# Kernel optimization log

Hardware: AMD Instinct MI355X
Metric: run time of the kernel (lower is better)

The kernel has to match this reference:

```python
import jax, jax.numpy as jnp
import numpy as np

SEQ = 2048
D_MODEL = 2048
N_HEAD = 16
D_QK = 128
D_V = 128
THETA = 10000.0


def setup_inputs() -> dict:
    key = jax.random.key(0)
    kx, kq, kk, kv, ko = jax.random.split(key, 5)
    x = jax.random.normal(kx, (SEQ, D_MODEL), dtype=jnp.float32)
    q = jax.random.normal(kq, (N_HEAD, D_MODEL, D_QK), dtype=jnp.float32)
    k = jax.random.normal(kk, (N_HEAD, D_MODEL, D_QK), dtype=jnp.float32)
    v = jax.random.normal(kv, (N_HEAD, D_MODEL, D_V), dtype=jnp.float32)
    o = jax.random.normal(ko, (N_HEAD, D_V, D_MODEL), dtype=jnp.float32)
    theta_factor = jnp.asarray(THETA, dtype=jnp.float32)
    return {"x": x, "q": q, "k": k, "v": v, "o": o, "theta_factor": theta_factor}


def _rope_embed(x, d_qk, theta_factor):
    # x: [..., S, d]. Rotate-half RoPE with frequencies theta^(-i/d_rope),
    # then scale by d_qk^(-1/4) so q.k gets the usual 1/sqrt(d_qk).
    S, d = x.shape[-2], x.shape[-1]
    d_rope = d // 2
    rates = theta_factor ** (-jnp.arange(d_rope, dtype=x.dtype) / d_rope)  # [d_rope]
    ang = jnp.arange(S, dtype=x.dtype)[:, None] * rates[None, :]           # [S, d_rope]
    sin, cos = jnp.sin(ang), jnp.cos(ang)
    x1, x2 = x[..., :d_rope], x[..., d_rope:]
    y = jnp.concatenate([cos * x1 - sin * x2, sin * x1 + cos * x2], axis=-1)
    return y * (d_qk ** -0.25)


def reference(x, q, k, v, o, theta_factor):
    # x: [S, D]; q,k: [H, D, d_qk]; v: [H, D, d_v]; o: [H, d_v, D]
    S = x.shape[0]
    d_qk = q.shape[2]
    qs = jnp.einsum('sd,hde->hse', x, q)   # [H, S, d_qk]
    ks = jnp.einsum('sd,hde->hse', x, k)   # [H, S, d_qk]
    vs = jnp.einsum('sd,hde->hse', x, v)   # [H, S, d_v]
    rq = _rope_embed(qs, d_qk, theta_factor)
    rk = _rope_embed(ks, d_qk, theta_factor)
    scores = jnp.einsum('hse,hte->hst', rq, rk)  # [H, S, S]
    causal = jnp.tril(jnp.ones((S, S), dtype=bool))
    scores = jnp.where(causal[None], scores, -jnp.inf)
    w = jax.nn.softmax(scores, axis=-1)
    y = jnp.einsum('hst,hte->hse', w, vs)        # [H, S, d_v]
    z = jnp.einsum('hse,hed->sd', y, o)          # [S, D] (sum over heads)
    return z
```

## Files before the change

kernel.cpp:

```cpp
#include <hip/hip_runtime.h>
#include <hip/hip_bf16.h>

#define SEQ 2048
#define DM  2048
#define NH  16
#define DE  128
#define DR  64
#define LDT 72
#define LDK 136

typedef __attribute__((ext_vector_type(8))) short bf16x8;
typedef __attribute__((ext_vector_type(4))) float f32x4;

#define VMCNT_WAIT(n) asm volatile("s_waitcnt vmcnt(" #n ")" ::: "memory")
#define CFENCE() asm volatile("" ::: "memory")

__device__ __forceinline__ unsigned short f2bf(float f) {
  unsigned u = __float_as_uint(f);
  u += 0x7fff + ((u >> 16) & 1);
  return (unsigned short)(u >> 16);
}
__device__ __forceinline__ float bf2f(unsigned short h) {
  return __uint_as_float((unsigned)h << 16);
}

__device__ __forceinline__ void gld16(const unsigned short* g, unsigned short* l) {
  __builtin_amdgcn_global_load_lds(
      (const __attribute__((address_space(1))) unsigned int*)g,
      (__attribute__((address_space(3))) unsigned int*)l, 16, 0, 0);
}

__global__ void k_split(const float* __restrict__ in, unsigned short* __restrict__ hi,
                        unsigned short* __restrict__ lo, int n4) {
  int i = blockIdx.x * blockDim.x + threadIdx.x;
  int stride = gridDim.x * blockDim.x;
  for (int idx = i; idx < n4; idx += stride) {
    float4 v = ((const float4*)in)[idx];
    ushort4 h, l;
    h.x = f2bf(v.x); l.x = f2bf(v.x - bf2f(h.x));
    h.y = f2bf(v.y); l.y = f2bf(v.y - bf2f(h.y));
    h.z = f2bf(v.z); l.z = f2bf(v.z - bf2f(h.z));
    h.w = f2bf(v.w); l.w = f2bf(v.w - bf2f(h.w));
    ((ushort4*)hi)[idx] = h;
    ((ushort4*)lo)[idx] = l;
  }
}

__global__ void k_transpose_split(const float* __restrict__ in, unsigned short* __restrict__ hi,
                                  unsigned short* __restrict__ lo, int rows, int cols) {
  __shared__ float tile[32][33];
  size_t bo = (size_t)blockIdx.z * rows * cols;
  int r0 = blockIdx.y * 32, c0 = blockIdx.x * 32;
  int tx = threadIdx.x, ty = threadIdx.y;
  #pragma unroll
  for (int i = 0; i < 32; i += 8)
    tile[ty + i][tx] = in[bo + (size_t)(r0 + ty + i) * cols + (c0 + tx)];
  __syncthreads();
  #pragma unroll
  for (int i = 0; i < 32; i += 8) {
    float v = tile[tx][ty + i];
    unsigned short h = f2bf(v);
    size_t oidx = bo + (size_t)(c0 + ty + i) * rows + (r0 + tx);
    hi[oidx] = h;
    lo[oidx] = f2bf(v - bf2f(h));
  }
}

__global__ void k_transpose_one(const float* __restrict__ in, unsigned short* __restrict__ out,
                                int rows, int cols) {
  __shared__ float tile[32][33];
  size_t bo = (size_t)blockIdx.z * rows * cols;
  int r0 = blockIdx.y * 32, c0 = blockIdx.x * 32;
  int tx = threadIdx.x, ty = threadIdx.y;
  #pragma unroll
  for (int i = 0; i < 32; i += 8)
    tile[ty + i][tx] = in[bo + (size_t)(r0 + ty + i) * cols + (c0 + tx)];
  __syncthreads();
  #pragma unroll
  for (int i = 0; i < 32; i += 8)
    out[bo + (size_t)(c0 + ty + i) * rows + (r0 + tx)] = f2bf(tile[tx][ty + i]);
}

__global__ void k_rope_tables(const float* __restrict__ theta_p,
                              float* __restrict__ cost, float* __restrict__ sint) {
  int s = blockIdx.x, j = threadIdx.x;
  float theta = theta_p[0];
  float rate = powf(theta, -(float)j * (1.0f / (float)DR));
  float ang = (float)s * rate;
  cost[s * DR + j] = cosf(ang);
  sint[s * DR + j] = sinf(ang);
}

__launch_bounds__(256)
__global__ void k_projall(const unsigned short* __restrict__ xh, const unsigned short* __restrict__ xl,
                          const unsigned short* __restrict__ wqh, const unsigned short* __restrict__ wql,
                          const unsigned short* __restrict__ wkh, const unsigned short* __restrict__ wkl,
                          const unsigned short* __restrict__ wvh,
                          unsigned short* __restrict__ rqh, unsigned short* __restrict__ rql,
                          unsigned short* __restrict__ rkh, unsigned short* __restrict__ rkl,
                          unsigned short* __restrict__ vstt,
                          const float* __restrict__ cost, const float* __restrict__ sint) {
  __shared__ unsigned short Ahs[2][128 * 32];
  __shared__ unsigned short Als[2][128 * 32];
  __shared__ unsigned short Bhs[2][128 * 32];
  __shared__ unsigned short Bls[2][128 * 32];
  int mt = blockIdx.x;
  int mat = blockIdx.y >> 4, h = blockIdx.y & 15;
  bool split = (mat < 2);
  const unsigned short* wph = (mat == 0 ? wqh : (mat == 1 ? wkh : wvh)) + (size_t)h * DE * DM;
  const unsigned short* wpl = (mat == 0 ? wql : wkl) + (size_t)h * DE * DM;
  int m0 = mt * 128;
  int tid = threadIdx.x, lane = tid & 63, wid = tid >> 6;
  int wr = wid >> 1, wc = wid & 1;

  f32x4 zero = {0.f, 0.f, 0.f, 0.f};
  f32x4 acc[4][4];
  #pragma unroll
  for (int i = 0; i < 4; ++i)
    #pragma unroll
    for (int j = 0; j < 4; ++j) acc[i][j] = zero;

  auto STAGE = [&](int buf, int k0) {
    #pragma unroll
    for (int p = 0; p < 2; ++p) {
      int r = p * 64 + wid * 16 + (lane >> 2);
      int c = ((lane & 3) ^ ((r >> 1) & 3)) * 8;
      int ld = r * 32 + (lane & 3) * 8;
      gld16(&xh[(size_t)(m0 + r) * DM + k0 + c], &Ahs[buf][ld]);
      gld16(&wph[(size_t)r * DM + k0 + c], &Bhs[buf][ld]);
      if (split) {
        gld16(&xl[(size_t)(m0 + r) * DM + k0 + c], &Als[buf][ld]);
        gld16(&wpl[(size_t)r * DM + k0 + c], &Bls[buf][ld]);
      }
    }
  };

  const int NT = DM / 32;
  STAGE(0, 0);
  STAGE(1, 32);
  int cl_ = lane & 15;
  int chunk = lane >> 4;
  #pragma unroll 2
  for (int t = 0; t < NT; ++t) {
    int buf = t & 1;
    if (split) { VMCNT_WAIT(8); } else { VMCNT_WAIT(4); }
    __builtin_amdgcn_s_barrier();
    CFENCE();
    bf16x8 ah[4], al[4], bh[4], bl[4];
    #pragma unroll
    for (int mf = 0; mf < 4; ++mf) {
      int row = wr * 64 + mf * 16 + cl_;
      int off = row * 32 + ((chunk ^ ((row >> 1) & 3)) * 8);
      ah[mf] = *(const bf16x8*)&Ahs[buf][off];
      if (split) al[mf] = *(const bf16x8*)&Als[buf][off];
    }
    #pragma unroll
    for (int nf = 0; nf < 4; ++nf) {
      int nfi = wc * 2 + (nf & 1) + (nf >> 1) * 4;
      int row = nfi * 16 + cl_;
      int off = row * 32 + ((chunk ^ ((row >> 1) & 3)) * 8);
      bh[nf] = *(const bf16x8*)&Bhs[buf][off];
      if (split) bl[nf] = *(const bf16x8*)&Bls[buf][off];
    }
    if (split) {
      #pragma unroll
      for (int mf = 0; mf < 4; ++mf)
        #pragma unroll
        for (int nf = 0; nf < 4; ++nf) {
          acc[mf][nf] = __builtin_amdgcn_mfma_f32_16x16x32_bf16(ah[mf], bh[nf], acc[mf][nf], 0, 0, 0);
          acc[mf][nf] = __builtin_amdgcn_mfma_f32_16x16x32_bf16(al[mf], bh[nf], acc[mf][nf], 0, 0, 0);
          acc[mf][nf] = __builtin_amdgcn_mfma_f32_16x16x32_bf16(ah[mf], bl[nf], acc[mf][nf], 0, 0, 0);
        }
    } else {
      #pragma unroll
      for (int mf = 0; mf < 4; ++mf)
        #pragma unroll
        for (int nf = 0; nf < 4; ++nf)
          acc[mf][nf] = __builtin_amdgcn_mfma_f32_16x16x32_bf16(ah[mf], bh[nf], acc[mf][nf], 0, 0, 0);
    }
    CFENCE();
    __builtin_amdgcn_s_barrier();
    int kn = (t + 2 < NT) ? (t + 2) * 32 : (NT - 1) * 32;
    STAGE(buf, kn);
  }
  VMCNT_WAIT(0);

  int cl = lane & 15, rl = (lane >> 4) * 4;
  if (mat == 2) {
    #pragma unroll
    for (int mf = 0; mf < 4; ++mf)
      #pragma unroll
      for (int nf = 0; nf < 4; ++nf) {
        int nfi = wc * 2 + (nf & 1) + (nf >> 1) * 4;
        #pragma unroll
        for (int j = 0; j < 4; ++j) {
          int s = m0 + wr * 64 + mf * 16 + rl + j;
          int e = nfi * 16 + cl;
          vstt[((size_t)h * DE + e) * SEQ + s] = f2bf(acc[mf][nf][j]);
        }
      }
  } else {
    unsigned short* oh = (mat == 0) ? rqh : rkh;
    unsigned short* ol = (mat == 0) ? rql : rkl;
    const float qsc = 0.2973017787506803f;
    #pragma unroll
    for (int mf = 0; mf < 4; ++mf)
      #pragma unroll
      for (int nf = 0; nf < 2; ++nf)
        #pragma unroll
        for (int j = 0; j < 4; ++j) {
          int s = m0 + wr * 64 + mf * 16 + rl + j;
          int e = wc * 32 + (nf & 1) * 16 + cl;
          float x1 = acc[mf][nf][j];
          float x2 = acc[mf][nf + 2][j];
          float c  = cost[s * DR + e];
          float sn = sint[s * DR + e];
          float v1 = (c * x1 - sn * x2) * qsc;
          float v2 = (sn * x1 + c * x2) * qsc;
          size_t i1 = ((size_t)h * SEQ + s) * DE + e;
          size_t i2 = i1 + DR;
          unsigned short h1 = f2bf(v1), h2 = f2bf(v2);
          oh[i1] = h1; ol[i1] = f2bf(v1 - bf2f(h1));
          oh[i2] = h2; ol[i2] = f2bf(v2 - bf2f(h2));
        }
  }
}

#define LOADKV(t0)                                                        \
  pkh0 = *(const int4*)&Kh[(size_t)((t0) + sk_r     ) * DE + sk_c];       \
  pkh1 = *(const int4*)&Kh[(size_t)((t0) + sk_r + 16) * DE + sk_c];       \
  pkh2 = *(const int4*)&Kh[(size_t)((t0) + sk_r + 32) * DE + sk_c];       \
  pkh3 = *(const int4*)&Kh[(size_t)((t0) + sk_r + 48) * DE + sk_c];       \
  pkl0 = *(const int4*)&Kl[(size_t)((t0) + sk_r     ) * DE + sk_c];       \
  pkl1 = *(const int4*)&Kl[(size_t)((t0) + sk_r + 16) * DE + sk_c];       \
  pkl2 = *(const int4*)&Kl[(size_t)((t0) + sk_r + 32) * DE + sk_c];       \
  pkl3 = *(const int4*)&Kl[(size_t)((t0) + sk_r + 48) * DE + sk_c];       \
  pvv0 = *(const int4*)&Vt[(size_t)(sv_r     ) * SEQ + (t0) + sv_c];      \
  pvv1 = *(const int4*)&Vt[(size_t)(sv_r + 32) * SEQ + (t0) + sv_c];      \
  pvv2 = *(const int4*)&Vt[(size_t)(sv_r + 64) * SEQ + (t0) + sv_c];      \
  pvv3 = *(const int4*)&Vt[(size_t)(sv_r + 96) * SEQ + (t0) + sv_c];

#define STOREKV()                                                         \
  *(int4*)&Khi[(sk_r     ) * LDK + sk_c] = pkh0;                          \
  *(int4*)&Khi[(sk_r + 16) * LDK + sk_c] = pkh1;                          \
  *(int4*)&Khi[(sk_r + 32) * LDK + sk_c] = pkh2;                          \
  *(int4*)&Khi[(sk_r + 48) * LDK + sk_c] = pkh3;                          \
  *(int4*)&Klo[(sk_r     ) * LDK + sk_c] = pkl0;                          \
  *(int4*)&Klo[(sk_r + 16) * LDK + sk_c] = pkl1;                          \
  *(int4*)&Klo[(sk_r + 32) * LDK + sk_c] = pkl2;                          \
  *(int4*)&Klo[(sk_r + 48) * LDK + sk_c] = pkl3;                          \
  *(int4*)&Vtl[(sv_r     ) * LDT + sv_c] = pvv0;                          \
  *(int4*)&Vtl[(sv_r + 32) * LDT + sv_c] = pvv1;                          \
  *(int4*)&Vtl[(sv_r + 64) * LDT + sv_c] = pvv2;                          \
  *(int4*)&Vtl[(sv_r + 96) * LDT + sv_c] = pvv3;

__launch_bounds__(256, 2)
__global__ void k_attn(const unsigned short* __restrict__ rqh, const unsigned short* __restrict__ rql,
                       const unsigned short* __restrict__ rkh, const unsigned short* __restrict__ rkl,
                       const unsigned short* __restrict__ vstt,
                       unsigned short* __restrict__ yb) {
  __shared__ unsigned short Khi[64 * LDK];
  __shared__ unsigned short Klo[64 * LDK];
  __shared__ unsigned short Vtl[128 * LDT];
  __shared__ unsigned short Pl[64 * LDT];
  int bid = blockIdx.x;
  int g = bid >> 4;
  int qt = (g < 16) ? (31 - g) : (g - 16);
  int h  = bid & 15;
  int m0 = qt * 64;
  int tid = threadIdx.x, lane = tid & 63, wid = tid >> 6;
  const unsigned short* Qh = rqh + (size_t)h * SEQ * DE;
  const unsigned short* Ql = rql + (size_t)h * SEQ * DE;
  const unsigned short* Kh = rkh + (size_t)h * SEQ * DE;
  const unsigned short* Kl = rkl + (size_t)h * SEQ * DE;
  const unsigned short* Vt = vstt + (size_t)h * DE * SEQ;
  int cl = lane & 15, hi = lane >> 4;

  bf16x8 qfh[4], qfl[4];
  {
    int qrow = m0 + wid * 16 + cl;
    #pragma unroll
    for (int ks = 0; ks < 4; ++ks) {
      qfh[ks] = *(const bf16x8*)&Qh[(size_t)qrow * DE + ks * 32 + hi * 8];
      qfl[ks] = *(const bf16x8*)&Ql[(size_t)qrow * DE + ks * 32 + hi * 8];
    }
  }

  f32x4 zero = {0.f, 0.f, 0.f, 0.f};
  f32x4 acc[8];
  #pragma unroll
  for (int nf = 0; nf < 8; ++nf) acc[nf] = zero;
  float mrow[4], lrow[4];
  #pragma unroll
  for (int j = 0; j < 4; ++j) { mrow[j] = -3e38f; lrow[j] = 0.f; }

  int sk_r = tid >> 4, sk_c = (tid & 15) * 8;
  int sv_r = tid >> 3, sv_c = (tid & 7) * 8;

  int4 pkh0, pkh1, pkh2, pkh3, pkl0, pkl1, pkl2, pkl3, pvv0, pvv1, pvv2, pvv3;

  int ntiles = qt + 1;
  LOADKV(0)
  for (int t = 0; t < ntiles; ++t) {
    int t0 = t * 64;
    STOREKV()
    __syncthreads();
    if (t + 1 < ntiles) { LOADKV(t0 + 64) }

    f32x4 sacc[4];
    #pragma unroll
    for (int tf = 0; tf < 4; ++tf) sacc[tf] = zero;
    __builtin_amdgcn_s_setprio(1);
    #pragma unroll
    for (int ks = 0; ks < 4; ++ks) {
      int kk = ks * 32 + hi * 8;
      #pragma unroll
      for (int tf = 0; tf < 4; ++tf) {
        int r = (tf * 16 + cl) * LDK + kk;
        bf16x8 bh = *(const bf16x8*)&Khi[r];
        bf16x8 bl = *(const bf16x8*)&Klo[r];
        sacc[tf] = __builtin_amdgcn_mfma_f32_16x16x32_bf16(qfh[ks], bh, sacc[tf], 0, 0, 0);
        sacc[tf] = __builtin_amdgcn_mfma_f32_16x16x32_bf16(qfl[ks], bh, sacc[tf], 0, 0, 0);
        sacc[tf] = __builtin_amdgcn_mfma_f32_16x16x32_bf16(qfh[ks], bl, sacc[tf], 0, 0, 0);
      }
    }
    __builtin_amdgcn_s_setprio(0);
    if (t == ntiles - 1) {
      int sb = m0 + wid * 16 + hi * 4;
      #pragma unroll
      for (int tf = 0; tf < 4; ++tf) {
        int tc = t0 + tf * 16 + cl;
        #pragma unroll
        for (int j = 0; j < 4; ++j)
          if (tc > sb + j) sacc[tf][j] = -3e38f;
      }
    }
    #pragma unroll
    for (int j = 0; j < 4; ++j) {
      float mx = fmaxf(fmaxf(sacc[0][j], sacc[1][j]), fmaxf(sacc[2][j], sacc[3][j]));
      mx = fmaxf(mx, __shfl_xor(mx, 1));
      mx = fmaxf(mx, __shfl_xor(mx, 2));
      mx = fmaxf(mx, __shfl_xor(mx, 4));
      mx = fmaxf(mx, __shfl_xor(mx, 8));
      float mnew = fmaxf(mrow[j], mx);
      float sc = __expf(mrow[j] - mnew);
      float sum = 0.f;
      #pragma unroll
      for (int tf = 0; tf < 4; ++tf) {
        float p = __expf(sacc[tf][j] - mnew);
        sacc[tf][j] = p;
        sum += p;
      }
      sum += __shfl_xor(sum, 1);
      sum += __shfl_xor(sum, 2);
      sum += __shfl_xor(sum, 4);
      sum += __shfl_xor(sum, 8);
      lrow[j] = lrow[j] * sc + sum;
      mrow[j] = mnew;
      #pragma unroll
      for (int nf = 0; nf < 8; ++nf) acc[nf][j] *= sc;
    }
    #pragma unroll
    for (int tf = 0; tf < 4; ++tf)
      #pragma unroll
      for (int j = 0; j < 4; ++j)
        Pl[(wid * 16 + hi * 4 + j) * LDT + tf * 16 + cl] = f2bf(sacc[tf][j]);
    __builtin_amdgcn_s_setprio(1);
    #pragma unroll
    for (int ks = 0; ks < 2; ++ks) {
      int kk = ks * 32 + hi * 8;
      bf16x8 a = *(const bf16x8*)&Pl[(wid * 16 + cl) * LDT + kk];
      #pragma unroll
      for (int nf = 0; nf < 8; ++nf) {
        bf16x8 b = *(const bf16x8*)&Vtl[(nf * 16 + cl) * LDT + kk];
        acc[nf] = __builtin_amdgcn_mfma_f32_16x16x32_bf16(a, b, acc[nf], 0, 0, 0);
      }
    }
    __builtin_amdgcn_s_setprio(0);
    __syncthreads();
  }

  #pragma unroll
  for (int j = 0; j < 4; ++j) {
    float inv = 1.0f / lrow[j];
    #pragma unroll
    for (int nf = 0; nf < 8; ++nf) acc[nf][j] *= inv;
  }
  #pragma unroll
  for (int nf = 0; nf < 8; ++nf)
    #pragma unroll
    for (int j = 0; j < 4; ++j) {
      int s = m0 + wid * 16 + hi * 4 + j;
      int e = nf * 16 + cl;
      yb[(size_t)s * DM + h * DE + e] = f2bf(acc[nf][j]);
    }
}

__launch_bounds__(256)
__global__ void k_out(const unsigned short* __restrict__ yb,
                      const unsigned short* __restrict__ otb,
                      float* __restrict__ z) {
  __shared__ unsigned short Ahs[2][128 * 32];
  __shared__ unsigned short Bhs[2][128 * 32];
  int m0 = blockIdx.x * 128, n0 = blockIdx.y * 128;
  int tid = threadIdx.x, lane = tid & 63, wid = tid >> 6;
  int wr = wid >> 1, wc = wid & 1;
  f32x4 zero = {0.f, 0.f, 0.f, 0.f};
  f32x4 acc[4][4];
  #pragma unroll
  for (int i = 0; i < 4; ++i)
    #pragma unroll
    for (int j = 0; j < 4; ++j) acc[i][j] = zero;

  auto STAGE = [&](int buf, int k0) {
    #pragma unroll
    for (int p = 0; p < 2; ++p) {
      int r = p * 64 + wid * 16 + (lane >> 2);
      int c = ((lane & 3) ^ ((r >> 1) & 3)) * 8;
      int ld = r * 32 + (lane & 3) * 8;
      gld16(&yb[(size_t)(m0 + r) * DM + k0 + c], &Ahs[buf][ld]);
      gld16(&otb[(size_t)(n0 + r) * DM + k0 + c], &Bhs[buf][ld]);
    }
  };

  const int NT = DM / 32;
  STAGE(0, 0);
  STAGE(1, 32);
  int cl_ = lane & 15;
  int chunk = lane >> 4;
  #pragma unroll 2
  for (int t = 0; t < NT; ++t) {
    int buf = t & 1;
    VMCNT_WAIT(4);
    __builtin_amdgcn_s_barrier();
    CFENCE();
    bf16x8 a[4], b[4];
    #pragma unroll
    for (int mf = 0; mf < 4; ++mf) {
      int row = wr * 64 + mf * 16 + cl_;
      a[mf] = *(const bf16x8*)&Ahs[buf][row * 32 + ((chunk ^ ((row >> 1) & 3)) * 8)];
    }
    #pragma unroll
    for (int nf = 0; nf < 4; ++nf) {
      int nfi = wc * 2 + (nf & 1) + (nf >> 1) * 4;
      int row = nfi * 16 + cl_;
      b[nf] = *(const bf16x8*)&Bhs[buf][row * 32 + ((chunk ^ ((row >> 1) & 3)) * 8)];
    }
    #pragma unroll
    for (int mf = 0; mf < 4; ++mf)
      #pragma unroll
      for (int nf = 0; nf < 4; ++nf)
        acc[mf][nf] = __builtin_amdgcn_mfma_f32_16x16x32_bf16(a[mf], b[nf], acc[mf][nf], 0, 0, 0);
    CFENCE();
    __builtin_amdgcn_s_barrier();
    int kn = (t + 2 < NT) ? (t + 2) * 32 : (NT - 1) * 32;
    STAGE(buf, kn);
  }
  VMCNT_WAIT(0);

  int cl = lane & 15, rl = (lane >> 4) * 4;
  #pragma unroll
  for (int mf = 0; mf < 4; ++mf)
    #pragma unroll
    for (int nf = 0; nf < 4; ++nf) {
      int nfi = wc * 2 + (nf & 1) + (nf >> 1) * 4;
      #pragma unroll
      for (int j = 0; j < 4; ++j) {
        int s = m0 + wr * 64 + mf * 16 + rl + j;
        int d = n0 + nfi * 16 + cl;
        z[(size_t)s * DM + d] = acc[mf][nf][j];
      }
    }
}

extern "C" void kernel_launch(void* const* d_in, const int* in_sizes, int n_in,
                              void* d_out, int out_size, void* d_ws, size_t ws_size,
                              hipStream_t stream) {
  const float* x  = (const float*)d_in[0];
  const float* q  = (const float*)d_in[1];
  const float* k  = (const float*)d_in[2];
  const float* v  = (const float*)d_in[3];
  const float* o  = (const float*)d_in[4];
  const float* th = (const float*)d_in[5];
  float* z = (float*)d_out;
  char* ws = (char*)d_ws;
  const size_t MB = 1024 * 1024;
  unsigned short* xh  = (unsigned short*)(ws);
  unsigned short* xl  = (unsigned short*)(ws + 8 * MB);
  unsigned short* wqh = (unsigned short*)(ws + 16 * MB);
  unsigned short* wql = (unsigned short*)(ws + 24 * MB);
  unsigned short* wkh = (unsigned short*)(ws + 32 * MB);
  unsigned short* wkl = (unsigned short*)(ws + 40 * MB);
  unsigned short* wvh = (unsigned short*)(ws + 48 * MB);
  unsigned short* rqh = (unsigned short*)(ws + 56 * MB);
  unsigned short* rql = (unsigned short*)(ws + 64 * MB);
  unsigned short* rkh = (unsigned short*)(ws + 72 * MB);
  unsigned short* rkl = (unsigned short*)(ws + 80 * MB);
  unsigned short* vst = (unsigned short*)(ws + 88 * MB);
  float* cost = (float*)(ws + 96 * MB);
  float* sint = (float*)(ws + 96 * MB + 512 * 1024);
  unsigned short* yb  = (unsigned short*)(ws + 16 * MB);
  unsigned short* otb = (unsigned short*)(ws + 24 * MB);

  dim3 tb(32, 8);
  k_rope_tables<<<SEQ, DR, 0, stream>>>(th, cost, sint);
  k_split<<<2048, 256, 0, stream>>>(x, xh, xl, SEQ * DM / 4);
  k_transpose_split<<<dim3(DE / 32, DM / 32, NH), tb, 0, stream>>>(q, wqh, wql, DM, DE);
  k_transpose_split<<<dim3(DE / 32, DM / 32, NH), tb, 0, stream>>>(k, wkh, wkl, DM, DE);
  k_transpose_one<<<dim3(DE / 32, DM / 32, NH), tb, 0, stream>>>(v, wvh, DM, DE);
  k_projall<<<dim3(16, 48), 256, 0, stream>>>(xh, xl, wqh, wql, wkh, wkl, wvh,
                                              rqh, rql, rkh, rkl, vst, cost, sint);
  k_transpose_one<<<dim3(DM / 32, (NH * DE) / 32, 1), tb, 0, stream>>>(o, otb, NH * DE, DM);
  k_attn<<<512, 256, 0, stream>>>(rqh, rql, rkh, rkl, vst, yb);
  k_out<<<dim3(16, 16), 256, 0, stream>>>(yb, otb, z);
}
```

Before: 318.2 us.

## Use 256x256 tiles with 8 waves and phased MFMA/LDS schedule in projection

The QKV projection GEMM moves from 128x128 tiles with 4 waves (768 blocks) to 256x256 tiles with 8 waves (192 blocks). Each wave now computes a 128x64 sub-tile in four phases that interleave LDS fragment reads, next-tile global prefetch and MFMA bursts, with barriers between phases and raised wave priority during the MFMA bursts. The larger tiles cut redundant global and LDS traffic per flop. In exchange the launch has only 192 blocks for 256 CUs, the loop waits for all outstanding loads each step and adds many barriers, and the 128 KB of LDS may not fit two blocks per CU.

```diff
diff --git a/kernel.cpp b/kernel.cpp
--- a/kernel.cpp
+++ b/kernel.cpp
@@ -91,8 +91,8 @@
   sint[s * DR + j] = sinf(ang);
 }
 
-__launch_bounds__(256)
-__global__ void k_projall(const unsigned short* __restrict__ xh, const unsigned short* __restrict__ xl,
+__launch_bounds__(512, 2)
+__global__ void k_proj256(const unsigned short* __restrict__ xh, const unsigned short* __restrict__ xl,
                           const unsigned short* __restrict__ wqh, const unsigned short* __restrict__ wql,
                           const unsigned short* __restrict__ wkh, const unsigned short* __restrict__ wkl,
                           const unsigned short* __restrict__ wvh,
@@ -100,103 +100,115 @@
                           unsigned short* __restrict__ rkh, unsigned short* __restrict__ rkl,
                           unsigned short* __restrict__ vstt,
                           const float* __restrict__ cost, const float* __restrict__ sint) {
-  __shared__ unsigned short Ahs[2][128 * 32];
-  __shared__ unsigned short Als[2][128 * 32];
-  __shared__ unsigned short Bhs[2][128 * 32];
-  __shared__ unsigned short Bls[2][128 * 32];
-  int mt = blockIdx.x;
-  int mat = blockIdx.y >> 4, h = blockIdx.y & 15;
+  __shared__ unsigned short Ahs[2][256 * 32];
+  __shared__ unsigned short Als[2][256 * 32];
+  __shared__ unsigned short Bhs[2][256 * 32];
+  __shared__ unsigned short Bls[2][256 * 32];
+  int bid = blockIdx.x;
+  int mat = bid >> 6;
+  int mt = (bid >> 3) & 7, nt = bid & 7;
   bool split = (mat < 2);
-  const unsigned short* wph = (mat == 0 ? wqh : (mat == 1 ? wkh : wvh)) + (size_t)h * DE * DM;
-  const unsigned short* wpl = (mat == 0 ? wql : wkl) + (size_t)h * DE * DM;
-  int m0 = mt * 128;
+  const unsigned short* wh = (mat == 0 ? wqh : (mat == 1 ? wkh : wvh));
+  const unsigned short* wl = (mat == 0 ? wql : wkl);
+  int m0 = mt * 256, n0 = nt * 256;
   int tid = threadIdx.x, lane = tid & 63, wid = tid >> 6;
-  int wr = wid >> 1, wc = wid & 1;
+  int wr = wid >> 2, wc = wid & 3;
+  int cl_ = lane & 15, chunk = lane >> 4;
+  int sr = tid >> 2, ss = tid & 3;
 
   f32x4 zero = {0.f, 0.f, 0.f, 0.f};
-  f32x4 acc[4][4];
-  #pragma unroll
-  for (int i = 0; i < 4; ++i)
+  f32x4 acc[8][4];
+  #pragma unroll
+  for (int i = 0; i < 8; ++i)
     #pragma unroll
     for (int j = 0; j < 4; ++j) acc[i][j] = zero;
 
-  auto STAGE = [&](int buf, int k0) {
-    #pragma unroll
-    for (int p = 0; p < 2; ++p) {
-      int r = p * 64 + wid * 16 + (lane >> 2);
-      int c = ((lane & 3) ^ ((r >> 1) & 3)) * 8;
-      int ld = r * 32 + (lane & 3) * 8;
-      gld16(&xh[(size_t)(m0 + r) * DM + k0 + c], &Ahs[buf][ld]);
-      gld16(&wph[(size_t)r * DM + k0 + c], &Bhs[buf][ld]);
-      if (split) {
-        gld16(&xl[(size_t)(m0 + r) * DM + k0 + c], &Als[buf][ld]);
-        gld16(&wpl[(size_t)r * DM + k0 + c], &Bls[buf][ld]);
-      }
-    }
-  };
-
+#define STAGEP(bufv, k0, p) {                                              \
+    int r_ = sr + (p) * 128;                                               \
+    int c_ = (ss ^ ((r_ >> 1) & 3)) * 8;                                   \
+    int ld_ = r_ * 32 + ss * 8;                                            \
+    gld16(&xh[(size_t)(m0 + r_) * DM + (k0) + c_], &Ahs[bufv][ld_]);       \
+    gld16(&wh[(size_t)(n0 + r_) * DM + (k0) + c_], &Bhs[bufv][ld_]);       \
+    if (split) {                                                           \
+      gld16(&xl[(size_t)(m0 + r_) * DM + (k0) + c_], &Als[bufv][ld_]);     \
+      gld16(&wl[(size_t)(n0 + r_) * DM + (k0) + c_], &Bls[bufv][ld_]);     \
+    }                                                                      \
+  }
+#define RA(dh, dl, mfv) {                                                  \
+    int row_ = wr * 128 + (mfv) * 16 + cl_;                                \
+    int off_ = row_ * 32 + ((chunk ^ ((row_ >> 1) & 3)) * 8);              \
+    dh = *(const bf16x8*)&Ahs[buf][off_];                                  \
+    if (split) dl = *(const bf16x8*)&Als[buf][off_];                       \
+  }
+#define RB(dh, dl, nfv) {                                                  \
+    int row_ = ((nfv) * 4 + wc) * 16 + cl_;                                \
+    int off_ = row_ * 32 + ((chunk ^ ((row_ >> 1) & 3)) * 8);              \
+    dh = *(const bf16x8*)&Bhs[buf][off_];                                  \
+    if (split) dl = *(const bf16x8*)&Bls[buf][off_];                       \
+  }
+#define MM3(a_, ahv, alv, bhv, blv)                                        \
+    a_ = __builtin_amdgcn_mfma_f32_16x16x32_bf16(ahv, bhv, a_, 0, 0, 0);   \
+    a_ = __builtin_amdgcn_mfma_f32_16x16x32_bf16(alv, bhv, a_, 0, 0, 0);   \
+    a_ = __builtin_amdgcn_mfma_f32_16x16x32_bf16(ahv, blv, a_, 0, 0, 0);
+#define MM1(a_, ahv, bhv)                                                  \
+    a_ = __builtin_amdgcn_mfma_f32_16x16x32_bf16(ahv, bhv, a_, 0, 0, 0);
+#define PH_MFMA(mA, mB, nA, nB)                                            \
+    __builtin_amdgcn_s_setprio(1);                                         \
+    if (split) {                                                           \
+      MM3(acc[mA][nA], ah0, al0, bh0, bl0) MM3(acc[mA][nB], ah0, al0, bh1, bl1) \
+      MM3(acc[mA+1][nA], ah1, al1, bh0, bl0) MM3(acc[mA+1][nB], ah1, al1, bh1, bl1) \
+      MM3(acc[mA+2][nA], ah2, al2, bh0, bl0) MM3(acc[mA+2][nB], ah2, al2, bh1, bl1) \
+      MM3(acc[mA+3][nA], ah3, al3, bh0, bl0) MM3(acc[mA+3][nB], ah3, al3, bh1, bl1) \
+    } else {                                                               \
+      MM1(acc[mA][nA], ah0, bh0) MM1(acc[mA][nB], ah0, bh1)                \
+      MM1(acc[mA+1][nA], ah1, bh0) MM1(acc[mA+1][nB], ah1, bh1)            \
+      MM1(acc[mA+2][nA], ah2, bh0) MM1(acc[mA+2][nB], ah2, bh1)            \
+      MM1(acc[mA+3][nA], ah3, bh0) MM1(acc[mA+3][nB], ah3, bh1)            \
+    }                                                                      \
+    __builtin_amdgcn_s_setprio(0);
+#define PBAR() CFENCE(); __builtin_amdgcn_s_barrier(); CFENCE();
+
+  STAGEP(0, 0, 0)
+  STAGEP(0, 0, 1)
   const int NT = DM / 32;
-  STAGE(0, 0);
-  STAGE(1, 32);
-  int cl_ = lane & 15;
-  int chunk = lane >> 4;
-  #pragma unroll 2
   for (int t = 0; t < NT; ++t) {
     int buf = t & 1;
-    if (split) { VMCNT_WAIT(8); } else { VMCNT_WAIT(4); }
-    __builtin_amdgcn_s_barrier();
-    CFENCE();
-    bf16x8 ah[4], al[4], bh[4], bl[4];
-    #pragma unroll
-    for (int mf = 0; mf < 4; ++mf) {
-      int row = wr * 64 + mf * 16 + cl_;
-      int off = row * 32 + ((chunk ^ ((row >> 1) & 3)) * 8);
-      ah[mf] = *(const bf16x8*)&Ahs[buf][off];
-      if (split) al[mf] = *(const bf16x8*)&Als[buf][off];
-    }
-    #pragma unroll
-    for (int nf = 0; nf < 4; ++nf) {
-      int nfi = wc * 2 + (nf & 1) + (nf >> 1) * 4;
-      int row = nfi * 16 + cl_;
-      int off = row * 32 + ((chunk ^ ((row >> 1) & 3)) * 8);
-      bh[nf] = *(const bf16x8*)&Bhs[buf][off];
-      if (split) bl[nf] = *(const bf16x8*)&Bls[buf][off];
-    }
-    if (split) {
-      #pragma unroll
-      for (int mf = 0; mf < 4; ++mf)
-        #pragma unroll
-        for (int nf = 0; nf < 4; ++nf) {
-          acc[mf][nf] = __builtin_amdgcn_mfma_f32_16x16x32_bf16(ah[mf], bh[nf], acc[mf][nf], 0, 0, 0);
-          acc[mf][nf] = __builtin_amdgcn_mfma_f32_16x16x32_bf16(al[mf], bh[nf], acc[mf][nf], 0, 0, 0);
-          acc[mf][nf] = __builtin_amdgcn_mfma_f32_16x16x32_bf16(ah[mf], bl[nf], acc[mf][nf], 0, 0, 0);
-        }
-    } else {
-      #pragma unroll
-      for (int mf = 0; mf < 4; ++mf)
-        #pragma unroll
-        for (int nf = 0; nf < 4; ++nf)
-          acc[mf][nf] = __builtin_amdgcn_mfma_f32_16x16x32_bf16(ah[mf], bh[nf], acc[mf][nf], 0, 0, 0);
-    }
-    CFENCE();
-    __builtin_amdgcn_s_barrier();
-    int kn = (t + 2 < NT) ? (t + 2) * 32 : (NT - 1) * 32;
-    STAGE(buf, kn);
+    VMCNT_WAIT(0);
+    PBAR();
+    bf16x8 ah0, ah1, ah2, ah3, al0, al1, al2, al3, bh0, bh1, bl0, bl1;
+    RA(ah0, al0, 0) RA(ah1, al1, 1) RA(ah2, al2, 2) RA(ah3, al3, 3)
+    RB(bh0, bl0, 0) RB(bh1, bl1, 1)
+    if (t + 1 < NT) STAGEP(buf ^ 1, (t + 1) * 32, 0)
+    PBAR();
+    PH_MFMA(0, 0, 0, 1)
+    PBAR();
+    RB(bh0, bl0, 2) RB(bh1, bl1, 3)
+    if (t + 1 < NT) STAGEP(buf ^ 1, (t + 1) * 32, 1)
+    PBAR();
+    PH_MFMA(0, 0, 2, 3)
+    PBAR();
+    RA(ah0, al0, 4) RA(ah1, al1, 5) RA(ah2, al2, 6) RA(ah3, al3, 7)
+    PBAR();
+    PH_MFMA(4, 4, 2, 3)
+    PBAR();
+    RB(bh0, bl0, 0) RB(bh1, bl1, 1)
+    PBAR();
+    PH_MFMA(4, 4, 0, 1)
+    PBAR();
   }
   VMCNT_WAIT(0);
 
   int cl = lane & 15, rl = (lane >> 4) * 4;
   if (mat == 2) {
     #pragma unroll
-    for (int mf = 0; mf < 4; ++mf)
+    for (int mf = 0; mf < 8; ++mf)
       #pragma unroll
       for (int nf = 0; nf < 4; ++nf) {
-        int nfi = wc * 2 + (nf & 1) + (nf >> 1) * 4;
+        int n = n0 + (nf * 4 + wc) * 16 + cl;
         #pragma unroll
         for (int j = 0; j < 4; ++j) {
-          int s = m0 + wr * 64 + mf * 16 + rl + j;
-          int e = nfi * 16 + cl;
-          vstt[((size_t)h * DE + e) * SEQ + s] = f2bf(acc[mf][nf][j]);
+          int s = m0 + wr * 128 + mf * 16 + rl + j;
+          vstt[(size_t)n * SEQ + s] = f2bf(acc[mf][nf][j]);
         }
       }
   } else {
@@ -204,26 +216,35 @@
     unsigned short* ol = (mat == 0) ? rql : rkl;
     const float qsc = 0.2973017787506803f;
     #pragma unroll
-    for (int mf = 0; mf < 4; ++mf)
-      #pragma unroll
-      for (int nf = 0; nf < 2; ++nf)
+    for (int mf = 0; mf < 8; ++mf)
+      #pragma unroll
+      for (int nfp = 0; nfp < 2; ++nfp) {
+        int hh = nt * 2 + nfp;
+        int e = wc * 16 + cl;
         #pragma unroll
         for (int j = 0; j < 4; ++j) {
-          int s = m0 + wr * 64 + mf * 16 + rl + j;
-          int e = wc * 32 + (nf & 1) * 16 + cl;
-          float x1 = acc[mf][nf][j];
-          float x2 = acc[mf][nf + 2][j];
+          int s = m0 + wr * 128 + mf * 16 + rl + j;
+          float x1 = acc[mf][nfp * 2][j];
+          float x2 = acc[mf][nfp * 2 + 1][j];
           float c  = cost[s * DR + e];
           float sn = sint[s * DR + e];
           float v1 = (c * x1 - sn * x2) * qsc;
           float v2 = (sn * x1 + c * x2) * qsc;
-          size_t i1 = ((size_t)h * SEQ + s) * DE + e;
+          size_t i1 = ((size_t)hh * SEQ + s) * DE + e;
           size_t i2 = i1 + DR;
           unsigned short h1 = f2bf(v1), h2 = f2bf(v2);
           oh[i1] = h1; ol[i1] = f2bf(v1 - bf2f(h1));
           oh[i2] = h2; ol[i2] = f2bf(v2 - bf2f(h2));
         }
-  }
+      }
+  }
+#undef STAGEP
+#undef RA
+#undef RB
+#undef MM3
+#undef MM1
+#undef PH_MFMA
+#undef PBAR
 }
 
 #define LOADKV(t0)                                                        \
@@ -508,8 +529,8 @@
   k_transpose_split<<<dim3(DE / 32, DM / 32, NH), tb, 0, stream>>>(q, wqh, wql, DM, DE);
   k_transpose_split<<<dim3(DE / 32, DM / 32, NH), tb, 0, stream>>>(k, wkh, wkl, DM, DE);
   k_transpose_one<<<dim3(DE / 32, DM / 32, NH), tb, 0, stream>>>(v, wvh, DM, DE);
-  k_projall<<<dim3(16, 48), 256, 0, stream>>>(xh, xl, wqh, wql, wkh, wkl, wvh,
-                                              rqh, rql, rkh, rkl, vst, cost, sint);
+  k_proj256<<<192, 512, 0, stream>>>(xh, xl, wqh, wql, wkh, wkl, wvh,
+                                     rqh, rql, rkh, rkl, vst, cost, sint);
   k_transpose_one<<<dim3(DM / 32, (NH * DE) / 32, 1), tb, 0, stream>>>(o, otb, NH * DE, DM);
   k_attn<<<512, 256, 0, stream>>>(rqh, rql, rkh, rkl, vst, yb);
   k_out<<<dim3(16, 16), 256, 0, stream>>>(yb, otb, z);
```

Result: slower. 356.1 us (+11.9%).
